# Kernel optimization log

Hardware: AMD Instinct MI355X
Metric: run time of the kernel (lower is better)

## Reference

```python
import jax, jax.numpy as jnp
import numpy as np

N = 500000      # examples = M * (nr+1)
K = 20          # context set size (indices[:, 3:])
NR = 24         # negatives per positive
H = 128         # hidden_channels == node feature dim
NODES = 10000   # ingredient vocabulary


def setup_inputs() -> dict:
    key = jax.random.key(0)
    ks = jax.random.split(key, 6)
    indices = jax.random.randint(ks[0], (N, 3 + K), 0, NODES)
    x = jax.random.normal(ks[1], (NODES, H), dtype=jnp.float32)
    scale = 0.02
    W1 = jax.random.normal(ks[2], (H, 3 * H), dtype=jnp.float32) * scale
    b1 = jnp.zeros((H,), jnp.float32)
    W2 = jax.random.normal(ks[3], (H // 2, H), dtype=jnp.float32) * scale
    b2 = jnp.zeros((H // 2,), jnp.float32)
    W3 = jax.random.normal(ks[4], (1, H // 2), dtype=jnp.float32) * scale
    b3 = jnp.zeros((1,), jnp.float32)
    return {"indices": indices, "nr": NR, "x": x,
            "W1": W1, "b1": b1, "W2": W2, "b2": b2, "W3": W3, "b3": b3}


def _embed_context(ctx_idx, x, nr):
    # ctx_idx: [N, K]; one context row per group of (nr+1) examples
    new_idx = ctx_idx[:-1:nr + 1]                 # [M, K]
    emb = x[new_idx]                               # [M, K, H] gather
    s = emb.sum(axis=1)                            # [M, H]
    norm = jnp.maximum((new_idx > 0).sum(axis=1), 1).astype(x.dtype)[:, None]
    mean = s / norm                                # masked mean over context
    return jnp.repeat(mean, nr + 1, axis=0)        # broadcast back to [N, H]


def reference(indices, nr, x, W1, b1, W2, b2, W3, b3):
    ing1 = x[indices[:, 0]]                        # [N, H]
    ing2 = x[indices[:, 1]]                        # [N, H]
    set_emb = _embed_context(indices[:, 3:], x, nr)  # [N, H]
    y = jnp.concatenate([ing1, ing2, set_emb], axis=1)  # [N, 3H]
    y = jax.nn.relu(y @ W1.T + b1)
    y = jax.nn.relu(y @ W2.T + b2)
    return y @ W3.T + b3                           # [N, 1]
```

## Files before the change

kernel.cpp:

```cpp
#include <hip/hip_runtime.h>
#include <hip/hip_bf16.h>

#define N_ROWS   500000
#define NR1      25
#define NGROUPS  20000
#define KCTX     20
#define H        128
#define NODES    10000
#define IDX_COLS 23

typedef __attribute__((ext_vector_type(8))) short short8;
typedef __attribute__((ext_vector_type(4))) float f32x4;

__device__ __forceinline__ unsigned pkbf(float lo, float hi) {
  __hip_bfloat162 h = __float22bfloat162_rn(make_float2(lo, hi));
  union { __hip_bfloat162 h; unsigned u; } c; c.h = h;
  return c.u;
}
__device__ __forceinline__ float lo2f(unsigned u) {
  union { unsigned u; float f; } c; c.u = u << 16; return c.f;
}
__device__ __forceinline__ float hi2f(unsigned u) {
  union { unsigned u; float f; } c; c.u = u & 0xffff0000u; return c.f;
}

#define PN 64
#define PBLK  ((NODES + PN - 1) / PN)
#define B_W2F (6 * PBLK)
#define PRE_BLOCKS (B_W2F + 1)

__global__ __launch_bounds__(256) void k_precompute(
    const float* __restrict__ x, const float* __restrict__ W1,
    const float* __restrict__ W2,
    unsigned short* __restrict__ Pb, unsigned short* __restrict__ w2f) {
  const int tid = threadIdx.x;
  const int bid = blockIdx.x;

  const int lane = tid & 63;
  const int wvid = tid >> 6;
  const int col  = lane & 15;
  const int quad = lane >> 4;

  if (bid == B_W2F) {
#pragma unroll
    for (int i = 0; i < 4; ++i) {
      const int fi = i * 4 + wvid;
      const int kt = fi >> 2, ct = fi & 3;
      const float* __restrict__ src =
          W2 + (size_t)(ct * 16 + col) * H + kt * 32 + quad * 8;
      const float4 v0 = *(const float4*)src;
      const float4 v1 = *(const float4*)(src + 4);
      union { short8 v; unsigned u[4]; } pk;
      pk.u[0] = pkbf(v0.x, v0.y);
      pk.u[1] = pkbf(v0.z, v0.w);
      pk.u[2] = pkbf(v1.x, v1.y);
      pk.u[3] = pkbf(v1.z, v1.w);
      *(short8*)(w2f + (size_t)(fi * 64 + lane) * 8) = pk.v;
    }
    return;
  }

  __shared__ __align__(16) short wlds[64 * 128];

  const int m   = bid / (2 * PBLK);
  const int sub = bid - m * (2 * PBLK);
  const int mcol = (m == 2) ? 2 : m;
  const int tbase = (sub >> 1) * PN;
  const int ch    = sub & 1;

#pragma unroll
  for (int it = 0; it < 8; ++it) {
    const int f  = it * 256 + tid;
    const int j  = f >> 5;
    const int q4 = f & 31;
    const float4 v =
        *(const float4*)(W1 + (size_t)(ch * 64 + j) * (3 * H) + mcol * H + q4 * 4);
    const int sidx = j * 128 + (((q4 >> 1) ^ (j & 7)) << 3) + (q4 & 1) * 4;
    *(unsigned*)&wlds[sidx]     = pkbf(v.x, v.y);
    *(unsigned*)&wlds[sidx + 2] = pkbf(v.z, v.w);
  }
  __syncthreads();

  int node = tbase + wvid * 16 + col;
  if (node > NODES - 1) node = NODES - 1;
  const float4* __restrict__ xr = (const float4*)(x + (size_t)node * H);
  short8 Af[4];
#pragma unroll
  for (int kt = 0; kt < 4; ++kt) {
    const int f4 = kt * 8 + quad * 2;
    const float4 v0 = xr[f4], v1 = xr[f4 + 1];
    union { short8 v; unsigned u[4]; } pk;
    pk.u[0] = pkbf(v0.x, v0.y);
    pk.u[1] = pkbf(v0.z, v0.w);
    pk.u[2] = pkbf(v1.x, v1.y);
    pk.u[3] = pkbf(v1.z, v1.w);
    Af[kt] = pk.v;
  }

  f32x4 acc[4];
#pragma unroll
  for (int ct = 0; ct < 4; ++ct) acc[ct] = (f32x4)(0.f);

#pragma unroll
  for (int kt = 0; kt < 4; ++kt) {
#pragma unroll
    for (int ct = 0; ct < 4; ++ct) {
      const int brow = ct * 16 + col;
      const short8 Bf = *(const short8*)
          &wlds[brow * 128 + (((kt * 4 + quad) ^ (brow & 7)) << 3)];
      acc[ct] = __builtin_amdgcn_mfma_f32_16x16x32_bf16(Af[kt], Bf, acc[ct], 0, 0, 0);
    }
  }

  unsigned short* __restrict__ Pm = Pb + (size_t)m * NODES * H;
#pragma unroll
  for (int reg = 0; reg < 4; ++reg) {
    const int n = tbase + wvid * 16 + quad * 4 + reg;
    if (n < NODES) {
#pragma unroll
      for (int ct = 0; ct < 4; ++ct) {
        union { unsigned u; unsigned short s[2]; } c;
        c.u = pkbf(acc[ct][reg], 0.f);
        Pm[(size_t)n * H + ch * 64 + ct * 16 + col] = c.s[0];
      }
    }
  }
}

#define GPB 8
#define CTX_BLOCKS (NGROUPS / GPB)
__global__ __launch_bounds__(256) void k_ctx(
    const int* __restrict__ indices, const unsigned short* __restrict__ P3b,
    const float* __restrict__ b1, unsigned short* __restrict__ Pgb) {
  const int tid  = threadIdx.x;
  const int sub  = tid >> 6;
  const int lane = tid & 63;
  const int jj   = lane * 2;
  const float2 b1v = *(const float2*)(b1 + jj);
#pragma unroll
  for (int it = 0; it < GPB / 4; ++it) {
    const int g = blockIdx.x * GPB + it * 4 + sub;
    const int* __restrict__ rowidx =
        indices + (size_t)g * NR1 * IDX_COLS + 3;
    float s0 = 0.f, s1 = 0.f;
    int cnt = 0;
#pragma unroll
    for (int c = 0; c < KCTX; ++c) {
      const int idx = rowidx[c];
      const unsigned w = *(const unsigned*)(P3b + (size_t)idx * H + jj);
      s0 += lo2f(w); s1 += hi2f(w);
      cnt += (idx > 0) ? 1 : 0;
    }
    const float rn = 1.f / (float)((cnt > 1) ? cnt : 1);
    *(unsigned*)(Pgb + (size_t)g * H + jj) = pkbf(b1v.x + s0 * rn, b1v.y + s1 * rn);
  }
}

#define RPW 32
__global__ __launch_bounds__(256, 4) void k_main(
    const int* __restrict__ indices,
    const unsigned short* __restrict__ P1b, const unsigned short* __restrict__ P2b,
    const unsigned short* __restrict__ Pgb, const unsigned short* __restrict__ w2f,
    const float* __restrict__ b2, const float* __restrict__ W3,
    const float* __restrict__ b3, float* __restrict__ out) {
  __shared__ __align__(16) short w2s[16 * 64 * 8];

  const int tid  = threadIdx.x;
  const int lane = tid & 63;
  const int wv   = tid >> 6;
  const int col  = lane & 15;
  const int quad = lane >> 4;

  {
    const short8* __restrict__ src = (const short8*)w2f;
    short8* dst = (short8*)w2s;
#pragma unroll
    for (int i = 0; i < 4; ++i) dst[i * 256 + tid] = src[i * 256 + tid];
  }
  __syncthreads();

  const int Rw = (blockIdx.x * 4 + wv) * RPW;
  const int r0 = Rw + col, r1 = Rw + 16 + col;
  const int rc0 = (r0 < N_ROWS) ? r0 : (N_ROWS - 1);
  const int rc1 = (r1 < N_ROWS) ? r1 : (N_ROWS - 1);
  const int g0 = rc0 / NR1, g1 = rc1 / NR1;

  const short8* __restrict__ pc0 = (const short8*)(Pgb + (size_t)g0 * H);
  const short8* __restrict__ pc1 = (const short8*)(Pgb + (size_t)g1 * H);
  short8 uc0[4], uc1[4];
#pragma unroll
  for (int kt = 0; kt < 4; ++kt) {
    uc0[kt] = pc0[kt * 4 + quad];
    uc1[kt] = pc1[kt * 4 + quad];
  }

  const int2 iA = *(const int2*)(indices + (size_t)rc0 * IDX_COLS);
  const int2 iB = *(const int2*)(indices + (size_t)rc1 * IDX_COLS);

  const short8* __restrict__ pa0 = (const short8*)(P1b + (size_t)iA.x * H);
  const short8* __restrict__ pb0 = (const short8*)(P2b + (size_t)iA.y * H);
  const short8* __restrict__ pa1 = (const short8*)(P1b + (size_t)iB.x * H);
  const short8* __restrict__ pb1 = (const short8*)(P2b + (size_t)iB.y * H);
  short8 ua0[4], ub0[4], ua1[4], ub1[4];
#pragma unroll
  for (int kt = 0; kt < 4; ++kt) {
    ua0[kt] = pa0[kt * 4 + quad];
    ub0[kt] = pb0[kt * 4 + quad];
    ua1[kt] = pa1[kt * 4 + quad];
    ub1[kt] = pb1[kt * 4 + quad];
  }
  __builtin_amdgcn_sched_barrier(0);

  float b2v[4], w3v[4];
#pragma unroll
  for (int ct = 0; ct < 4; ++ct) {
    b2v[ct] = b2[ct * 16 + col];
    w3v[ct] = W3[ct * 16 + col];
  }
  const float bias3 = b3[0];

  short8 A0[4], A1[4];
#pragma unroll
  for (int kt = 0; kt < 4; ++kt) {
    union { short8 v; unsigned u[4]; } va, vb, vc;
    va.v = ua0[kt]; vb.v = ub0[kt]; vc.v = uc0[kt];
    union { short8 v; unsigned u[4]; } pk;
#pragma unroll
    for (int w = 0; w < 4; ++w) {
      const float hl = fmaxf(lo2f(va.u[w]) + lo2f(vb.u[w]) + lo2f(vc.u[w]), 0.f);
      const float hh = fmaxf(hi2f(va.u[w]) + hi2f(vb.u[w]) + hi2f(vc.u[w]), 0.f);
      pk.u[w] = pkbf(hl, hh);
    }
    A0[kt] = pk.v;
  }
#pragma unroll
  for (int kt = 0; kt < 4; ++kt) {
    union { short8 v; unsigned u[4]; } va, vb, vc;
    va.v = ua1[kt]; vb.v = ub1[kt]; vc.v = uc1[kt];
    union { short8 v; unsigned u[4]; } pk;
#pragma unroll
    for (int w = 0; w < 4; ++w) {
      const float hl = fmaxf(lo2f(va.u[w]) + lo2f(vb.u[w]) + lo2f(vc.u[w]), 0.f);
      const float hh = fmaxf(hi2f(va.u[w]) + hi2f(vb.u[w]) + hi2f(vc.u[w]), 0.f);
      pk.u[w] = pkbf(hl, hh);
    }
    A1[kt] = pk.v;
  }

  f32x4 acc0[4], acc1[4];
#pragma unroll
  for (int ct = 0; ct < 4; ++ct) { acc0[ct] = (f32x4)(0.f); acc1[ct] = (f32x4)(0.f); }
#pragma unroll
  for (int kt = 0; kt < 4; ++kt) {
#pragma unroll
    for (int ct = 0; ct < 4; ++ct) {
      const short8 Bf = *(const short8*)&w2s[((kt * 4 + ct) * 64 + lane) * 8];
      acc0[ct] = __builtin_amdgcn_mfma_f32_16x16x32_bf16(A0[kt], Bf, acc0[ct], 0, 0, 0);
      acc1[ct] = __builtin_amdgcn_mfma_f32_16x16x32_bf16(A1[kt], Bf, acc1[ct], 0, 0, 0);
    }
  }

#pragma unroll
  for (int grp = 0; grp < 2; ++grp) {
#pragma unroll
    for (int reg = 0; reg < 4; ++reg) {
      float s = 0.f;
#pragma unroll
      for (int ct = 0; ct < 4; ++ct) {
        const float a = (grp == 0) ? acc0[ct][reg] : acc1[ct][reg];
        s += fmaxf(a + b2v[ct], 0.f) * w3v[ct];
      }
      s += __shfl_xor(s, 1);
      s += __shfl_xor(s, 2);
      s += __shfl_xor(s, 4);
      s += __shfl_xor(s, 8);
      if (col == 0) {
        const int row = Rw + grp * 16 + quad * 4 + reg;
        if (row < N_ROWS) out[row] = s + bias3;
      }
    }
  }
}

extern "C" void kernel_launch(void* const* d_in, const int* in_sizes, int n_in,
                              void* d_out, int out_size, void* d_ws, size_t ws_size,
                              hipStream_t stream) {
  const int*   indices = (const int*)  d_in[0];
  const float* x  = (const float*)d_in[2];
  const float* W1 = (const float*)d_in[3];
  const float* b1 = (const float*)d_in[4];
  const float* W2 = (const float*)d_in[5];
  const float* b2 = (const float*)d_in[6];
  const float* W3 = (const float*)d_in[7];
  const float* b3 = (const float*)d_in[8];
  float* out = (float*)d_out;

  unsigned short* Pb  = (unsigned short*)d_ws;
  unsigned short* P1b = Pb;
  unsigned short* P2b = Pb + (size_t)NODES * H;
  unsigned short* P3b = Pb + (size_t)2 * NODES * H;
  unsigned short* Pgb = Pb + (size_t)3 * NODES * H;
  unsigned short* w2f = Pgb + (size_t)NGROUPS * H;

  k_precompute<<<PRE_BLOCKS, 256, 0, stream>>>(x, W1, W2, Pb, w2f);
  k_ctx<<<CTX_BLOCKS, 256, 0, stream>>>(indices, P3b, b1, Pgb);
  k_main<<<(N_ROWS + 4 * RPW - 1) / (4 * RPW), 256, 0, stream>>>(
      indices, P1b, P2b, Pgb, w2f, b2, W3, b3, out);
}
```

Before: 149.8 us.

## Merge context-mean and projection into one pre-kernel, compact index pairs

Folds the context kernel into the precompute kernel. Each group's masked mean is now taken over raw fp32 x rows and then projected through W1's third block with MFMA, instead of projecting every node first and gathering the projected bf16 rows. The same launch also writes a compact int2 array of the first two index columns so the main kernel reads 8 contiguous bytes per row instead of strided 92-byte rows. This removes one launch and the P3 node projection, but the context gather now reads fp32 x rows, twice the bytes of the bf16 P3 rows, and adds an extra pass over indices.

Measured after the change: 164.6 us. +9.9%, slower.

```diff
diff --git a/kernel.cpp b/kernel.cpp
--- a/kernel.cpp
+++ b/kernel.cpp
@@ -25,140 +25,212 @@
 }
 
 #define PN 64
-#define PBLK  ((NODES + PN - 1) / PN)
-#define B_W2F (6 * PBLK)
-#define PRE_BLOCKS (B_W2F + 1)
-
-__global__ __launch_bounds__(256) void k_precompute(
-    const float* __restrict__ x, const float* __restrict__ W1,
+#define PBLK      ((NODES + PN - 1) / PN)
+#define B_PG_END  ((NGROUPS + 63) / 64)
+#define B_P12     B_PG_END
+#define B_IDXP    (B_P12 + 4 * PBLK)
+#define B_W2FP    (B_IDXP + PBLK)
+#define PRE_BLOCKS (B_W2FP + 1)
+
+__global__ __launch_bounds__(256) void k_pre(
+    const int* __restrict__ indices, const float* __restrict__ x,
+    const float* __restrict__ W1, const float* __restrict__ b1,
     const float* __restrict__ W2,
-    unsigned short* __restrict__ Pb, unsigned short* __restrict__ w2f) {
+    unsigned short* __restrict__ Pb, unsigned short* __restrict__ Pgb,
+    unsigned short* __restrict__ w2f, int2* __restrict__ idx2) {
+  __shared__ __align__(16) short lds_all[24576];
+
   const int tid = threadIdx.x;
   const int bid = blockIdx.x;
-
   const int lane = tid & 63;
   const int wvid = tid >> 6;
   const int col  = lane & 15;
   const int quad = lane >> 4;
 
-  if (bid == B_W2F) {
-#pragma unroll
-    for (int i = 0; i < 4; ++i) {
-      const int fi = i * 4 + wvid;
-      const int kt = fi >> 2, ct = fi & 3;
-      const float* __restrict__ src =
-          W2 + (size_t)(ct * 16 + col) * H + kt * 32 + quad * 8;
-      const float4 v0 = *(const float4*)src;
-      const float4 v1 = *(const float4*)(src + 4);
+  if (bid >= B_IDXP) {
+    if (bid == B_W2FP) {
+#pragma unroll
+      for (int i = 0; i < 4; ++i) {
+        const int fi = i * 4 + wvid;
+        const int kt = fi >> 2, ct = fi & 3;
+        const float* __restrict__ src =
+            W2 + (size_t)(ct * 16 + col) * H + kt * 32 + quad * 8;
+        const float4 v0 = *(const float4*)src;
+        const float4 v1 = *(const float4*)(src + 4);
+        union { short8 v; unsigned u[4]; } pk;
+        pk.u[0] = pkbf(v0.x, v0.y);
+        pk.u[1] = pkbf(v0.z, v0.w);
+        pk.u[2] = pkbf(v1.x, v1.y);
+        pk.u[3] = pkbf(v1.z, v1.w);
+        *(short8*)(w2f + (size_t)(fi * 64 + lane) * 8) = pk.v;
+      }
+    } else {
+      const int stride = PBLK * 256;
+      for (int r = (bid - B_IDXP) * 256 + tid; r < N_ROWS; r += stride)
+        idx2[r] = make_int2(indices[(size_t)r * IDX_COLS + 0],
+                            indices[(size_t)r * IDX_COLS + 1]);
+    }
+    return;
+  }
+
+  if (bid < B_PG_END) {
+    short* w13  = lds_all;
+    short* mlds = lds_all + 16384;
+    const int gbase = bid * 64;
+
+#pragma unroll
+    for (int it = 0; it < 16; ++it) {
+      const int f  = it * 256 + tid;
+      const int j  = f >> 5;
+      const int q4 = f & 31;
+      const float4 v = *(const float4*)(W1 + (size_t)j * (3 * H) + 2 * H + q4 * 4);
+      const int sidx = j * 128 + (((q4 >> 1) ^ (j & 7)) << 3) + (q4 & 1) * 4;
+      *(unsigned*)&w13[sidx]     = pkbf(v.x, v.y);
+      *(unsigned*)&w13[sidx + 2] = pkbf(v.z, v.w);
+    }
+
+    const int jj = lane * 2;
+#pragma unroll
+    for (int it = 0; it < 8; ++it) {
+      const int ga = gbase + wvid * 16 + it;
+      const int gb = ga + 8;
+      const int gac = (ga < NGROUPS) ? ga : (NGROUPS - 1);
+      const int gbc = (gb < NGROUPS) ? gb : (NGROUPS - 1);
+      const int* __restrict__ ra = indices + (size_t)gac * NR1 * IDX_COLS + 3;
+      const int* __restrict__ rb = indices + (size_t)gbc * NR1 * IDX_COLS + 3;
+      float a0 = 0.f, a1 = 0.f, c0 = 0.f, c1 = 0.f;
+      int ca = 0, cb = 0;
+#pragma unroll
+      for (int c = 0; c < KCTX; ++c) {
+        const int ia = ra[c], ib = rb[c];
+        const float2 va = *(const float2*)(x + (size_t)ia * H + jj);
+        const float2 vb = *(const float2*)(x + (size_t)ib * H + jj);
+        a0 += va.x; a1 += va.y; c0 += vb.x; c1 += vb.y;
+        ca += (ia > 0) ? 1 : 0; cb += (ib > 0) ? 1 : 0;
+      }
+      const float rna = 1.f / (float)((ca > 1) ? ca : 1);
+      const float rnb = 1.f / (float)((cb > 1) ? cb : 1);
+      {
+        const int row = wvid * 16 + it;
+        const int sb = row * 128 + (((lane >> 2) ^ (row & 7)) << 3) + (lane & 3) * 2;
+        *(unsigned*)&mlds[sb] = pkbf(a0 * rna, a1 * rna);
+      }
+      {
+        const int row = wvid * 16 + it + 8;
+        const int sb = row * 128 + (((lane >> 2) ^ (row & 7)) << 3) + (lane & 3) * 2;
+        *(unsigned*)&mlds[sb] = pkbf(c0 * rnb, c1 * rnb);
+      }
+    }
+    __syncthreads();
+
+    short8 Af[4];
+    const int arow = wvid * 16 + col;
+#pragma unroll
+    for (int kt = 0; kt < 4; ++kt)
+      Af[kt] = *(const short8*)
+          &mlds[arow * 128 + (((kt * 4 + quad) ^ (arow & 7)) << 3)];
+
+    f32x4 acc[8];
+#pragma unroll
+    for (int ct = 0; ct < 8; ++ct) acc[ct] = (f32x4)(0.f);
+#pragma unroll
+    for (int kt = 0; kt < 4; ++kt) {
+#pragma unroll
+      for (int ct = 0; ct < 8; ++ct) {
+        const int brow = ct * 16 + col;
+        const short8 Bf = *(const short8*)
+            &w13[brow * 128 + (((kt * 4 + quad) ^ (brow & 7)) << 3)];
+        acc[ct] = __builtin_amdgcn_mfma_f32_16x16x32_bf16(Af[kt], Bf, acc[ct], 0, 0, 0);
+      }
+    }
+    float b1v[8];
+#pragma unroll
+    for (int ct = 0; ct < 8; ++ct) b1v[ct] = b1[ct * 16 + col];
+#pragma unroll
+    for (int reg = 0; reg < 4; ++reg) {
+      const int g2 = gbase + wvid * 16 + quad * 4 + reg;
+      if (g2 < NGROUPS) {
+#pragma unroll
+        for (int ct = 0; ct < 8; ++ct) {
+          union { unsigned u; unsigned short s[2]; } c;
+          c.u = pkbf(acc[ct][reg] + b1v[ct], 0.f);
+          Pgb[(size_t)g2 * H + ct * 16 + col] = c.s[0];
+        }
+      }
+    }
+    return;
+  }
+
+  {
+    short* wlds = lds_all;
+    const int local = bid - B_P12;
+    const int m   = local / (2 * PBLK);
+    const int sub = local - m * (2 * PBLK);
+    const int tbase = (sub >> 1) * PN;
+    const int ch    = sub & 1;
+
+#pragma unroll
+    for (int it = 0; it < 8; ++it) {
+      const int f  = it * 256 + tid;
+      const int j  = f >> 5;
+      const int q4 = f & 31;
+      const float4 v =
+          *(const float4*)(W1 + (size_t)(ch * 64 + j) * (3 * H) + m * H + q4 * 4);
+      const int sidx = j * 128 + (((q4 >> 1) ^ (j & 7)) << 3) + (q4 & 1) * 4;
+      *(unsigned*)&wlds[sidx]     = pkbf(v.x, v.y);
+      *(unsigned*)&wlds[sidx + 2] = pkbf(v.z, v.w);
+    }
+    __syncthreads();
+
+    int node = tbase + wvid * 16 + col;
+    if (node > NODES - 1) node = NODES - 1;
+    const float4* __restrict__ xr = (const float4*)(x + (size_t)node * H);
+    short8 Af[4];
+#pragma unroll
+    for (int kt = 0; kt < 4; ++kt) {
+      const int f4 = kt * 8 + quad * 2;
+      const float4 v0 = xr[f4], v1 = xr[f4 + 1];
       union { short8 v; unsigned u[4]; } pk;
       pk.u[0] = pkbf(v0.x, v0.y);
       pk.u[1] = pkbf(v0.z, v0.w);
       pk.u[2] = pkbf(v1.x, v1.y);
       pk.u[3] = pkbf(v1.z, v1.w);
-      *(short8*)(w2f + (size_t)(fi * 64 + lane) * 8) = pk.v;
-    }
-    return;
-  }
-
-  __shared__ __align__(16) short wlds[64 * 128];
-
-  const int m   = bid / (2 * PBLK);
-  const int sub = bid - m * (2 * PBLK);
-  const int mcol = (m == 2) ? 2 : m;
-  const int tbase = (sub >> 1) * PN;
-  const int ch    = sub & 1;
-
-#pragma unroll
-  for (int it = 0; it < 8; ++it) {
-    const int f  = it * 256 + tid;
-    const int j  = f >> 5;
-    const int q4 = f & 31;
-    const float4 v =
-        *(const float4*)(W1 + (size_t)(ch * 64 + j) * (3 * H) + mcol * H + q4 * 4);
-    const int sidx = j * 128 + (((q4 >> 1) ^ (j & 7)) << 3) + (q4 & 1) * 4;
-    *(unsigned*)&wlds[sidx]     = pkbf(v.x, v.y);
-    *(unsigned*)&wlds[sidx + 2] = pkbf(v.z, v.w);
-  }
-  __syncthreads();
-
-  int node = tbase + wvid * 16 + col;
-  if (node > NODES - 1) node = NODES - 1;
-  const float4* __restrict__ xr = (const float4*)(x + (size_t)node * H);
-  short8 Af[4];
-#pragma unroll
-  for (int kt = 0; kt < 4; ++kt) {
-    const int f4 = kt * 8 + quad * 2;
-    const float4 v0 = xr[f4], v1 = xr[f4 + 1];
-    union { short8 v; unsigned u[4]; } pk;
-    pk.u[0] = pkbf(v0.x, v0.y);
-    pk.u[1] = pkbf(v0.z, v0.w);
-    pk.u[2] = pkbf(v1.x, v1.y);
-    pk.u[3] = pkbf(v1.z, v1.w);
-    Af[kt] = pk.v;
-  }
-
-  f32x4 acc[4];
-#pragma unroll
-  for (int ct = 0; ct < 4; ++ct) acc[ct] = (f32x4)(0.f);
-
-#pragma unroll
-  for (int kt = 0; kt < 4; ++kt) {
-#pragma unroll
-    for (int ct = 0; ct < 4; ++ct) {
-      const int brow = ct * 16 + col;
-      const short8 Bf = *(const short8*)
-          &wlds[brow * 128 + (((kt * 4 + quad) ^ (brow & 7)) << 3)];
-      acc[ct] = __builtin_amdgcn_mfma_f32_16x16x32_bf16(Af[kt], Bf, acc[ct], 0, 0, 0);
-    }
-  }
-
-  unsigned short* __restrict__ Pm = Pb + (size_t)m * NODES * H;
-#pragma unroll
-  for (int reg = 0; reg < 4; ++reg) {
-    const int n = tbase + wvid * 16 + quad * 4 + reg;
-    if (n < NODES) {
+      Af[kt] = pk.v;
+    }
+
+    f32x4 acc[4];
+#pragma unroll
+    for (int ct = 0; ct < 4; ++ct) acc[ct] = (f32x4)(0.f);
+#pragma unroll
+    for (int kt = 0; kt < 4; ++kt) {
 #pragma unroll
       for (int ct = 0; ct < 4; ++ct) {
-        union { unsigned u; unsigned short s[2]; } c;
-        c.u = pkbf(acc[ct][reg], 0.f);
-        Pm[(size_t)n * H + ch * 64 + ct * 16 + col] = c.s[0];
-      }
-    }
-  }
-}
-
-#define GPB 8
-#define CTX_BLOCKS (NGROUPS / GPB)
-__global__ __launch_bounds__(256) void k_ctx(
-    const int* __restrict__ indices, const unsigned short* __restrict__ P3b,
-    const float* __restrict__ b1, unsigned short* __restrict__ Pgb) {
-  const int tid  = threadIdx.x;
-  const int sub  = tid >> 6;
-  const int lane = tid & 63;
-  const int jj   = lane * 2;
-  const float2 b1v = *(const float2*)(b1 + jj);
-#pragma unroll
-  for (int it = 0; it < GPB / 4; ++it) {
-    const int g = blockIdx.x * GPB + it * 4 + sub;
-    const int* __restrict__ rowidx =
-        indices + (size_t)g * NR1 * IDX_COLS + 3;
-    float s0 = 0.f, s1 = 0.f;
-    int cnt = 0;
-#pragma unroll
-    for (int c = 0; c < KCTX; ++c) {
-      const int idx = rowidx[c];
-      const unsigned w = *(const unsigned*)(P3b + (size_t)idx * H + jj);
-      s0 += lo2f(w); s1 += hi2f(w);
-      cnt += (idx > 0) ? 1 : 0;
-    }
-    const float rn = 1.f / (float)((cnt > 1) ? cnt : 1);
-    *(unsigned*)(Pgb + (size_t)g * H + jj) = pkbf(b1v.x + s0 * rn, b1v.y + s1 * rn);
+        const int brow = ct * 16 + col;
+        const short8 Bf = *(const short8*)
+            &wlds[brow * 128 + (((kt * 4 + quad) ^ (brow & 7)) << 3)];
+        acc[ct] = __builtin_amdgcn_mfma_f32_16x16x32_bf16(Af[kt], Bf, acc[ct], 0, 0, 0);
+      }
+    }
+
+    unsigned short* __restrict__ Pm = Pb + (size_t)m * NODES * H;
+#pragma unroll
+    for (int reg = 0; reg < 4; ++reg) {
+      const int n = tbase + wvid * 16 + quad * 4 + reg;
+      if (n < NODES) {
+#pragma unroll
+        for (int ct = 0; ct < 4; ++ct) {
+          union { unsigned u; unsigned short s[2]; } c;
+          c.u = pkbf(acc[ct][reg], 0.f);
+          Pm[(size_t)n * H + ch * 64 + ct * 16 + col] = c.s[0];
+        }
+      }
+    }
   }
 }
 
 #define RPW 32
 __global__ __launch_bounds__(256, 4) void k_main(
-    const int* __restrict__ indices,
+    const int2* __restrict__ idx2,
     const unsigned short* __restrict__ P1b, const unsigned short* __restrict__ P2b,
     const unsigned short* __restrict__ Pgb, const unsigned short* __restrict__ w2f,
     const float* __restrict__ b2, const float* __restrict__ W3,
@@ -194,8 +266,8 @@
     uc1[kt] = pc1[kt * 4 + quad];
   }
 
-  const int2 iA = *(const int2*)(indices + (size_t)rc0 * IDX_COLS);
-  const int2 iB = *(const int2*)(indices + (size_t)rc1 * IDX_COLS);
+  const int2 iA = idx2[rc0];
+  const int2 iB = idx2[rc1];
 
   const short8* __restrict__ pa0 = (const short8*)(P1b + (size_t)iA.x * H);
   const short8* __restrict__ pb0 = (const short8*)(P2b + (size_t)iA.y * H);
@@ -298,12 +370,12 @@
   unsigned short* Pb  = (unsigned short*)d_ws;
   unsigned short* P1b = Pb;
   unsigned short* P2b = Pb + (size_t)NODES * H;
-  unsigned short* P3b = Pb + (size_t)2 * NODES * H;
-  unsigned short* Pgb = Pb + (size_t)3 * NODES * H;
+  unsigned short* Pgb = Pb + (size_t)2 * NODES * H;
   unsigned short* w2f = Pgb + (size_t)NGROUPS * H;
-
-  k_precompute<<<PRE_BLOCKS, 256, 0, stream>>>(x, W1, W2, Pb, w2f);
-  k_ctx<<<CTX_BLOCKS, 256, 0, stream>>>(indices, P3b, b1, Pgb);
+  int2* idx2 = (int2*)(w2f + 16 * 64 * 8);
+
+  k_pre<<<PRE_BLOCKS, 256, 0, stream>>>(indices, x, W1, b1, W2,
+                                        Pb, Pgb, w2f, idx2);
   k_main<<<(N_ROWS + 4 * RPW - 1) / (4 * RPW), 256, 0, stream>>>(
-      indices, P1b, P2b, Pgb, w2f, b2, W3, b3, out);
-}
+      idx2, P1b, P2b, Pgb, w2f, b2, W3, b3, out);
+}
```
